# Performance work log

Hardware: AMD Instinct MI355X
Metric: run time of the kernel (lower is better)

Reference implementation:

```python
import jax, jax.numpy as jnp
import numpy as np

N = 524288
NUM_LEVELS = 16
FEATS = 2
LOG2_T = 19
TABLE = 1 << LOG2_T
MIN_RES, MAX_RES = 16, 1024
PRIMES = np.array([1, 2654435761, 805459861], dtype=np.uint32)
_growth = np.exp((np.log(MAX_RES) - np.log(MIN_RES)) / (NUM_LEVELS - 1))
SCALINGS = np.floor(MIN_RES * _growth ** np.arange(NUM_LEVELS)).astype(np.float32)  # [L]


def hash_encode(positions, table):
    # positions [N,3] in [0,1]; table [L*T, F]
    scaled = positions[:, None, :] * jnp.asarray(SCALINGS)[None, :, None]  # [N,L,3]
    fl = jnp.floor(scaled)
    ce = jnp.ceil(scaled)
    offset = scaled - fl  # [N,L,3]
    primes = jnp.asarray(PRIMES)  # [3] uint32
    lvl_off = jnp.arange(NUM_LEVELS, dtype=jnp.uint32) * jnp.uint32(TABLE)  # [L]
    out = jnp.zeros(scaled.shape[:2] + (FEATS,), scaled.dtype)
    for corner in range(8):
        bits = np.array([(corner >> d) & 1 for d in range(3)], dtype=np.float32)
        coord = jnp.where(jnp.asarray(bits, dtype=bool), ce, fl)
        h = coord.astype(jnp.int32).astype(jnp.uint32) * primes  # [N,L,3]
        h = h[..., 0] ^ h[..., 1] ^ h[..., 2]
        idx = ((h & jnp.uint32(TABLE - 1)) + lvl_off).astype(jnp.int32)  # [N,L]
        b = jnp.asarray(bits)
        w = jnp.prod(b * offset + (1.0 - b) * (1.0 - offset), axis=-1, keepdims=True)  # [N,L,1]
        out = out + w * table[idx]
    return out.reshape(out.shape[0], NUM_LEVELS * FEATS)  # [N,32]


def nerf_encode(d):
    # NeRFEncoding: 4 freqs in 2**linspace(0,4,4), include_input=True -> 27 dims
    freqs = 2.0 ** jnp.linspace(0.0, 4.0, 4)
    scaled = (2.0 * jnp.pi * d)[..., None] * freqs  # [N,3,4]
    scaled = scaled.reshape(d.shape[0], -1)  # [N,12]
    enc = jnp.sin(jnp.concatenate([scaled, scaled + jnp.pi / 2.0], axis=-1))  # [N,24]
    return jnp.concatenate([enc, d], axis=-1)  # [N,27]


def setup_inputs() -> dict:
    key = jax.random.key(0)
    ks = jax.random.split(key, 16)
    w = lambda k, i, o: jax.random.normal(k, (i, o), jnp.float32) * (1.0 / np.sqrt(i))
    return {
        "positions": jax.random.uniform(ks[0], (N, 3), jnp.float32),
        "directions": jax.random.normal(ks[1], (N, 3), jnp.float32),
        "hash_table": (jax.random.uniform(ks[2], (NUM_LEVELS * TABLE, FEATS), jnp.float32) * 2.0 - 1.0) * 1e-3,
        "w0": w(ks[3], 32, 64), "b0": jnp.zeros((64,), jnp.float32),
        "w1": w(ks[4], 64, 64), "b1": jnp.zeros((64,), jnp.float32),
        "w2": w(ks[5], 64, 64), "b2": jnp.zeros((64,), jnp.float32),
        "wr": w(ks[6], 91, 32), "br": jnp.zeros((32,), jnp.float32),
        "wc": w(ks[7], 32, 3), "bc": jnp.zeros((3,), jnp.float32),
        "wd": w(ks[8], 64, 1), "bd": jnp.zeros((1,), jnp.float32),
    }


def reference(positions, directions, hash_table, w0, b0, w1, b1, w2, b2, wr, br, wc, bc, wd, bd):
    enc_xyz = hash_encode(positions, hash_table)  # [N,32]
    enc_dir = nerf_encode(directions)  # [N,27]
    h = jax.nn.relu(enc_xyz @ w0 + b0)
    h = jax.nn.relu(h @ w1 + b1)
    base = h @ w2 + b2  # [N,64], linear out (out_activation=None)
    rgb_h = jnp.concatenate([enc_dir, base], axis=-1) @ wr + br  # [N,32], single layer
    rgb = jax.nn.sigmoid(rgb_h @ wc + bc)  # [N,3]
    density = jax.nn.softplus(base @ wd + bd)  # [N,1]
    return jnp.concatenate([rgb, density], axis=-1)  # [N,4]
```

## Files before the change

### kernel.cpp

```cpp
#include <hip/hip_runtime.h>
#include <math.h>

#define NPTS 524288
#define LOG2T 19
#define TSIZE (1u << LOG2T)
#define TMASK (TSIZE - 1u)

typedef unsigned int uint32;
typedef unsigned short ushort16;

typedef __attribute__((ext_vector_type(8))) short short8;
typedef __attribute__((ext_vector_type(4))) float f32x4;

__device__ __forceinline__ float bf2f(ushort16 u) {
    union { uint32 i; float f; } v; v.i = ((uint32)u) << 16; return v.f;
}
__device__ __forceinline__ ushort16 f2bf(float f) {
    union { float f; uint32 i; } v; v.f = f;
    uint32 r = v.i + 0x7fffu + ((v.i >> 16) & 1u);
    return (ushort16)(r >> 16);
}
__device__ __forceinline__ uint32 pack2(float a, float b) {
    return (uint32)f2bf(a) | ((uint32)f2bf(b) << 16);
}
__device__ __forceinline__ float ldin(const void* p, int i, bool f32) {
    return f32 ? ((const float*)p)[i] : bf2f(((const ushort16*)p)[i]);
}

struct Scal16 { float s[16]; };
struct Freq4  { float f[4]; };

__global__ __launch_bounds__(256) void k_cvt(const void* __restrict__ pos,
                                             const float4* __restrict__ tbl,
                                             uint4* __restrict__ tbl2) {
    __shared__ int sFlag;
    int tid = threadIdx.x;
    if (tid < 64) {
        const ushort16* ph = (const ushort16*)pos;
        float v0 = bf2f(ph[tid]), v1 = bf2f(ph[tid + 64]);
        bool odd = !(fabsf(v0) <= 4.f) || !(fabsf(v1) <= 4.f);
        unsigned long long m = __ballot(odd);
        if (tid == 0) sFlag = (m != 0ull) ? 1 : 0;
    }
    __syncthreads();
    if (sFlag == 0) return;
    size_t g = (size_t)blockIdx.x * 256 + tid;
    float4 v0 = tbl[2 * g], v1 = tbl[2 * g + 1];
    uint4 o;
    o.x = pack2(v0.x, v0.y); o.y = pack2(v0.z, v0.w);
    o.z = pack2(v1.x, v1.y); o.w = pack2(v1.z, v1.w);
    tbl2[g] = o;
}

__global__ __launch_bounds__(256) void k_hash2(const void* __restrict__ pos,
                                               const void* __restrict__ tbl,
                                               const uint32* __restrict__ tbl2,
                                               uint32* __restrict__ enc,
                                               Scal16 sc, int lvl0) {
    __shared__ int sFlag;
    int tid = threadIdx.x;
    if (tid < 64) {
        const ushort16* ph = (const ushort16*)pos;
        float v0 = bf2f(ph[tid]), v1 = bf2f(ph[tid + 64]);
        bool odd = !(fabsf(v0) <= 4.f) || !(fabsf(v1) <= 4.f);
        unsigned long long m = __ballot(odd);
        if (tid == 0) sFlag = (m != 0ull) ? 1 : 0;
    }
    __syncthreads();
    const bool f32 = (sFlag != 0);
    const uint32* tp = f32 ? tbl2 : (const uint32*)tbl;

    int lvl = lvl0 + (blockIdx.x & 7);
    int pt = (blockIdx.x >> 3) * 256 + tid;

    float s = sc.s[lvl];
    float x = ldin(pos, 3 * pt, f32), y = ldin(pos, 3 * pt + 1, f32), z = ldin(pos, 3 * pt + 2, f32);
    float sx = x * s, sy = y * s, sz = z * s;
    float fx = floorf(sx), fy = floorf(sy), fz = floorf(sz);
    float cx = ceilf(sx), cy = ceilf(sy), cz = ceilf(sz);
    float ox = sx - fx, oy = sy - fy, oz = sz - fz;
    uint32 hx0 = (uint32)(int)fx;
    uint32 hx1 = (uint32)(int)cx;
    uint32 hy0 = (uint32)(int)fy * 2654435761u;
    uint32 hy1 = (uint32)(int)cy * 2654435761u;
    uint32 hz0 = (uint32)(int)fz * 805459861u;
    uint32 hz1 = (uint32)(int)cz * 805459861u;
    uint32 base = (uint32)lvl << LOG2T;
    float wx0 = 1.f - ox, wy0 = 1.f - oy, wz0 = 1.f - oz;

    float a0 = 0.f, a1 = 0.f;
#pragma unroll
    for (int yz = 0; yz < 4; ++yz) {
        uint32 m = ((yz & 1) ? hy1 : hy0) ^ ((yz & 2) ? hz1 : hz0);
        float wyz = ((yz & 1) ? oy : wy0) * ((yz & 2) ? oz : wz0);
        uint32 i0 = ((hx0 ^ m) & TMASK) + base;
        uint32 i1 = ((hx1 ^ m) & TMASK) + base;
        uint32 d0, d1;
        if (i1 == (i0 ^ 1u)) {
            uint2 pv = *(const uint2*)(tp + (i0 & ~1u));
            d0 = (i0 & 1u) ? pv.y : pv.x;
            d1 = (i0 & 1u) ? pv.x : pv.y;
        } else {
            d0 = tp[i0]; d1 = tp[i1];
        }
        float f0 = bf2f((ushort16)(d0 & 0xffffu)), f1 = bf2f((ushort16)(d0 >> 16));
        float c0 = bf2f((ushort16)(d1 & 0xffffu)), c1 = bf2f((ushort16)(d1 >> 16));
        a0 += wyz * (wx0 * f0 + ox * c0);
        a1 += wyz * (wx0 * f1 + ox * c1);
    }
    enc[(size_t)lvl * NPTS + pt] = pack2(a0, a1);
}

__global__ __launch_bounds__(256) void k_hash(const void* __restrict__ pos,
                                              const void* __restrict__ tbl,
                                              uint32* __restrict__ enc,
                                              Scal16 sc) {
    __shared__ int sFlag;
    int tid = threadIdx.x;
    if (tid < 64) {
        const ushort16* ph = (const ushort16*)pos;
        float v0 = bf2f(ph[tid]), v1 = bf2f(ph[tid + 64]);
        bool odd = !(fabsf(v0) <= 4.f) || !(fabsf(v1) <= 4.f);
        unsigned long long m = __ballot(odd);
        if (tid == 0) sFlag = (m != 0ull) ? 1 : 0;
    }
    __syncthreads();
    const bool f32 = (sFlag != 0);

    int lvl = ((blockIdx.x >> 14) << 3) + (blockIdx.x & 7);
    int pt = ((blockIdx.x >> 3) & 2047) * 256 + tid;

    float s = sc.s[lvl];
    float x = ldin(pos, 3 * pt, f32), y = ldin(pos, 3 * pt + 1, f32), z = ldin(pos, 3 * pt + 2, f32);
    float sx = x * s, sy = y * s, sz = z * s;
    float fx = floorf(sx), fy = floorf(sy), fz = floorf(sz);
    float cx = ceilf(sx), cy = ceilf(sy), cz = ceilf(sz);
    float ox = sx - fx, oy = sy - fy, oz = sz - fz;
    uint32 hx0 = (uint32)(int)fx;
    uint32 hx1 = (uint32)(int)cx;
    uint32 hy0 = (uint32)(int)fy * 2654435761u;
    uint32 hy1 = (uint32)(int)cy * 2654435761u;
    uint32 hz0 = (uint32)(int)fz * 805459861u;
    uint32 hz1 = (uint32)(int)cz * 805459861u;
    uint32 base = (uint32)lvl << LOG2T;
    float wx0 = 1.f - ox, wy0 = 1.f - oy, wz0 = 1.f - oz;

    float a0 = 0.f, a1 = 0.f;
    if (f32) {
        const float* tf = (const float*)tbl;
#pragma unroll
        for (int yz = 0; yz < 4; ++yz) {
            uint32 m = ((yz & 1) ? hy1 : hy0) ^ ((yz & 2) ? hz1 : hz0);
            float wyz = ((yz & 1) ? oy : wy0) * ((yz & 2) ? oz : wz0);
            uint32 i0 = ((hx0 ^ m) & TMASK) + base;
            uint32 i1 = ((hx1 ^ m) & TMASK) + base;
            float4 pv = *(const float4*)(tf + (size_t)(i0 & ~1u) * 2);
            bool lo = !(i0 & 1u);
            float f0 = lo ? pv.x : pv.z, f1 = lo ? pv.y : pv.w;
            float c0, c1;
            if (i1 == (i0 ^ 1u)) { c0 = lo ? pv.z : pv.x; c1 = lo ? pv.w : pv.y; }
            else { float2 tv = ((const float2*)tbl)[i1]; c0 = tv.x; c1 = tv.y; }
            a0 += wyz * (wx0 * f0 + ox * c0);
            a1 += wyz * (wx0 * f1 + ox * c1);
        }
    } else {
#pragma unroll
        for (int cr = 0; cr < 8; ++cr) {
            uint32 h = ((cr & 1) ? hx1 : hx0) ^ ((cr & 2) ? hy1 : hy0) ^ ((cr & 4) ? hz1 : hz0);
            uint32 idx = (h & TMASK) + base;
            uint32 dv = ((const uint32*)tbl)[idx];
            float w = ((cr & 1) ? ox : wx0) * ((cr & 2) ? oy : wy0) * ((cr & 4) ? oz : wz0);
            a0 += w * bf2f((ushort16)(dv & 0xffffu));
            a1 += w * bf2f((ushort16)(dv >> 16));
        }
    }
    enc[(size_t)lvl * NPTS + pt] = pack2(a0, a1);
}

#define STRY 72
#define STRW0 40
#define STRW12 72
#define STRWR 104
#define MSTRX 100
#define PPI 128
#define NIT (NPTS / PPI)

__global__ __launch_bounds__(512) void k_mlp(
    const void* __restrict__ pos,
    const uint32* __restrict__ enc, const void* __restrict__ dirs,
    const void* __restrict__ w0, const void* __restrict__ b0,
    const void* __restrict__ w1, const void* __restrict__ b1,
    const void* __restrict__ w2, const void* __restrict__ b2,
    const void* __restrict__ wr, const void* __restrict__ br,
    const void* __restrict__ wc, const void* __restrict__ bc,
    const void* __restrict__ wd, const void* __restrict__ bd,
    void* __restrict__ out, Freq4 fq)
{
    __shared__ __align__(16) ushort16 sX[PPI * MSTRX];
    __shared__ __align__(16) ushort16 sY[PPI * STRY];
    __shared__ __align__(16) ushort16 sW0[64 * STRW0];
    __shared__ __align__(16) ushort16 sW1[64 * STRW12];
    __shared__ __align__(16) ushort16 sW2[64 * STRW12];
    __shared__ __align__(16) ushort16 sWR[32 * STRWR];
    __shared__ __align__(16) ushort16 sW4[16 * STRWR];
    __shared__ __align__(16) float sB0[64], sB1[64], sB2[64], sBR[32], sFB[4];
    __shared__ int sFlag;

    int tid = threadIdx.x;

    if (tid < 64) {
        const ushort16* ph = (const ushort16*)pos;
        float v0 = bf2f(ph[tid]), v1 = bf2f(ph[tid + 64]);
        bool odd = !(fabsf(v0) <= 4.f) || !(fabsf(v1) <= 4.f);
        unsigned long long m = __ballot(odd);
        if (tid == 0) sFlag = (m != 0ull) ? 1 : 0;
    }
    __syncthreads();
    const bool f32 = (sFlag != 0);

    for (int i = tid; i < 2048; i += 512) { int k = i >> 6, n = i & 63; sW0[n * STRW0 + k] = f2bf(ldin(w0, i, f32)); }
    for (int i = tid; i < 4096; i += 512) { int k = i >> 6, n = i & 63; sW1[n * STRW12 + k] = f2bf(ldin(w1, i, f32)); }
    for (int i = tid; i < 4096; i += 512) { int k = i >> 6, n = i & 63; sW2[n * STRW12 + k] = f2bf(ldin(w2, i, f32)); }
    for (int i = tid; i < 2912; i += 512) {
        int r = i >> 5, n = i & 31; int k = (r < 27) ? r : r + 5;
        sWR[n * STRWR + k] = f2bf(ldin(wr, i, f32));
    }
    if (tid < 160) { int n = tid / 5, k = 27 + tid % 5; sWR[n * STRWR + k] = 0; }
    for (int i = tid; i < 1536; i += 512) {
        int n = i / 96, j = i % 96;
        float v = 0.f;
        if (n == 3 && j < 64) v = ldin(wd, j, f32);
        else if (n < 3 && j >= 64) v = ldin(wc, (j - 64) * 3 + n, f32);
        sW4[n * STRWR + j] = f2bf(v);
    }
    if (tid < 64) { sB0[tid] = ldin(b0, tid, f32); sB1[tid] = ldin(b1, tid, f32); sB2[tid] = ldin(b2, tid, f32); }
    if (tid < 32) sBR[tid] = ldin(br, tid, f32);
    if (tid < 3) sFB[tid] = ldin(bc, tid, f32);
    if (tid == 3) sFB[3] = ldin(bd, 0, f32);

    int lane = tid & 63, wv = tid >> 6;
    int colg = lane & 15, quad = lane >> 4;
    int myrow = wv * 16 + colg;

    for (int c = blockIdx.x; c < NIT; c += gridDim.x) {
        int p0 = c * PPI;
        __syncthreads();

        for (int i = tid; i < 1024; i += 512) {
            int l = i >> 6, p2 = (i & 63) * 2;
            uint2 e = *(const uint2*)&enc[(size_t)l * NPTS + p0 + p2];
            *(uint32*)&sX[p2 * MSTRX + 2 * l] = e.x;
            *(uint32*)&sX[(p2 + 1) * MSTRX + 2 * l] = e.y;
        }
        if (tid < 384) {
            int p = tid / 3, i2 = tid - 3 * (tid / 3);
            float dvv = ldin(dirs, 3 * (p0 + p) + i2, f32);
            ushort16* row = &sX[p * MSTRX + 64];
            float td = 6.28318530717958647692f * dvv;
            float a0 = td * fq.f[0], a1 = td * fq.f[1], a2 = td * fq.f[2], a3 = td * fq.f[3];
            uint2 sv, cv;
            sv.x = pack2(__sinf(a0), __sinf(a1));
            sv.y = pack2(__sinf(a2), __sinf(a3));
            cv.x = pack2(__cosf(a0), __cosf(a1));
            cv.y = pack2(__cosf(a2), __cosf(a3));
            *(uint2*)&row[i2 * 4] = sv;
            *(uint2*)&row[12 + i2 * 4] = cv;
            row[24 + i2] = f2bf(dvv);
        } else {
            int p = tid - 384;
            ushort16* row = &sX[p * MSTRX + 64];
#pragma unroll
            for (int j = 27; j < 32; ++j) row[j] = 0;
        }
        __syncthreads();

        {
            short8 xb = *(const short8*)&sX[myrow * MSTRX + quad * 8];
#pragma unroll
            for (int nt = 0; nt < 4; ++nt) {
                short8 a = *(const short8*)&sW0[(nt * 16 + colg) * STRW0 + quad * 8];
                f32x4 acc = {0.f, 0.f, 0.f, 0.f};
                acc = __builtin_amdgcn_mfma_f32_16x16x32_bf16(a, xb, acc, 0, 0, 0);
                float4 bi = *(const float4*)&sB0[nt * 16 + quad * 4];
                uint2 o;
                o.x = pack2(fmaxf(acc[0] + bi.x, 0.f), fmaxf(acc[1] + bi.y, 0.f));
                o.y = pack2(fmaxf(acc[2] + bi.z, 0.f), fmaxf(acc[3] + bi.w, 0.f));
                *(uint2*)&sY[myrow * STRY + nt * 16 + quad * 4] = o;
            }
        }
        {
            short8 xb0 = *(const short8*)&sY[myrow * STRY + quad * 8];
            short8 xb1 = *(const short8*)&sY[myrow * STRY + 32 + quad * 8];
#pragma unroll
            for (int nt = 0; nt < 4; ++nt) {
                short8 a0 = *(const short8*)&sW1[(nt * 16 + colg) * STRW12 + quad * 8];
                short8 a1 = *(const short8*)&sW1[(nt * 16 + colg) * STRW12 + 32 + quad * 8];
                f32x4 acc = {0.f, 0.f, 0.f, 0.f};
                acc = __builtin_amdgcn_mfma_f32_16x16x32_bf16(a0, xb0, acc, 0, 0, 0);
                acc = __builtin_amdgcn_mfma_f32_16x16x32_bf16(a1, xb1, acc, 0, 0, 0);
                float4 bi = *(const float4*)&sB1[nt * 16 + quad * 4];
                uint2 o;
                o.x = pack2(fmaxf(acc[0] + bi.x, 0.f), fmaxf(acc[1] + bi.y, 0.f));
                o.y = pack2(fmaxf(acc[2] + bi.z, 0.f), fmaxf(acc[3] + bi.w, 0.f));
                *(uint2*)&sX[myrow * MSTRX + nt * 16 + quad * 4] = o;
            }
        }
        {
            short8 xb0 = *(const short8*)&sX[myrow * MSTRX + quad * 8];
            short8 xb1 = *(const short8*)&sX[myrow * MSTRX + 32 + quad * 8];
#pragma unroll
            for (int nt = 0; nt < 4; ++nt) {
                short8 a0 = *(const short8*)&sW2[(nt * 16 + colg) * STRW12 + quad * 8];
                short8 a1 = *(const short8*)&sW2[(nt * 16 + colg) * STRW12 + 32 + quad * 8];
                f32x4 acc = {0.f, 0.f, 0.f, 0.f};
                acc = __builtin_amdgcn_mfma_f32_16x16x32_bf16(a0, xb0, acc, 0, 0, 0);
                acc = __builtin_amdgcn_mfma_f32_16x16x32_bf16(a1, xb1, acc, 0, 0, 0);
                float4 bi = *(const float4*)&sB2[nt * 16 + quad * 4];
                uint2 o;
                o.x = pack2(acc[0] + bi.x, acc[1] + bi.y);
                o.y = pack2(acc[2] + bi.z, acc[3] + bi.w);
                *(uint2*)&sY[myrow * STRY + nt * 16 + quad * 4] = o;
            }
        }
        {
            short8 xb0 = *(const short8*)&sX[myrow * MSTRX + 64 + quad * 8];
            short8 xb1 = *(const short8*)&sY[myrow * STRY + quad * 8];
            short8 xb2 = *(const short8*)&sY[myrow * STRY + 32 + quad * 8];
#pragma unroll
            for (int nt = 0; nt < 2; ++nt) {
                short8 a0 = *(const short8*)&sWR[(nt * 16 + colg) * STRWR + quad * 8];
                short8 a1 = *(const short8*)&sWR[(nt * 16 + colg) * STRWR + 32 + quad * 8];
                short8 a2 = *(const short8*)&sWR[(nt * 16 + colg) * STRWR + 64 + quad * 8];
                f32x4 acc = {0.f, 0.f, 0.f, 0.f};
                acc = __builtin_amdgcn_mfma_f32_16x16x32_bf16(a0, xb0, acc, 0, 0, 0);
                acc = __builtin_amdgcn_mfma_f32_16x16x32_bf16(a1, xb1, acc, 0, 0, 0);
                acc = __builtin_amdgcn_mfma_f32_16x16x32_bf16(a2, xb2, acc, 0, 0, 0);
                float4 bi = *(const float4*)&sBR[nt * 16 + quad * 4];
                uint2 o;
                o.x = pack2(acc[0] + bi.x, acc[1] + bi.y);
                o.y = pack2(acc[2] + bi.z, acc[3] + bi.w);
                *(uint2*)&sX[myrow * MSTRX + nt * 16 + quad * 4] = o;
            }
        }
        {
            short8 xb0 = *(const short8*)&sY[myrow * STRY + quad * 8];
            short8 xb1 = *(const short8*)&sY[myrow * STRY + 32 + quad * 8];
            short8 xb2 = *(const short8*)&sX[myrow * MSTRX + quad * 8];
            short8 a0 = *(const short8*)&sW4[colg * STRWR + quad * 8];
            short8 a1 = *(const short8*)&sW4[colg * STRWR + 32 + quad * 8];
            short8 a2 = *(const short8*)&sW4[colg * STRWR + 64 + quad * 8];
            f32x4 acc = {0.f, 0.f, 0.f, 0.f};
            acc = __builtin_amdgcn_mfma_f32_16x16x32_bf16(a0, xb0, acc, 0, 0, 0);
            acc = __builtin_amdgcn_mfma_f32_16x16x32_bf16(a1, xb1, acc, 0, 0, 0);
            acc = __builtin_amdgcn_mfma_f32_16x16x32_bf16(a2, xb2, acc, 0, 0, 0);
            if (quad == 0) {
                float r0 = acc[0] + sFB[0], r1 = acc[1] + sFB[1], r2 = acc[2] + sFB[2], dd = acc[3] + sFB[3];
                r0 = 1.f / (1.f + expf(-r0));
                r1 = 1.f / (1.f + expf(-r1));
                r2 = 1.f / (1.f + expf(-r2));
                float sp = (dd > 0.f) ? (dd + log1pf(expf(-dd))) : log1pf(expf(dd));
                int pt = p0 + myrow;
                if (f32) {
                    float4 o4; o4.x = r0; o4.y = r1; o4.z = r2; o4.w = sp;
                    ((float4*)out)[pt] = o4;
                } else {
                    uint2 o; o.x = pack2(r0, r1); o.y = pack2(r2, sp);
                    ((uint2*)out)[pt] = o;
                }
            }
        }
    }
}

#define FSTRX 104
__global__ __launch_bounds__(256) void k_fused(
    const void* __restrict__ pos, const void* __restrict__ dirs,
    const void* __restrict__ tbl,
    const void* __restrict__ w0, const void* __restrict__ b0,
    const void* __restrict__ w1, const void* __restrict__ b1,
    const void* __restrict__ w2, const void* __restrict__ b2,
    const void* __restrict__ wr, const void* __restrict__ br,
    const void* __restrict__ wc, const void* __restrict__ bc,
    const void* __restrict__ wd, const void* __restrict__ bd,
    void* __restrict__ out, Scal16 sc, Freq4 fq)
{
    __shared__ __align__(16) ushort16 sX[64 * FSTRX];
    __shared__ __align__(16) ushort16 sY[64 * STRY];
    __shared__ __align__(16) ushort16 sW0[64 * STRW0];
    __shared__ __align__(16) ushort16 sW1[64 * STRW12];
    __shared__ __align__(16) ushort16 sW2[64 * STRW12];
    __shared__ __align__(16) ushort16 sWR[32 * STRWR];
    __shared__ float sB0[64], sB1[64], sB2[64], sBR[32];
    __shared__ float sWCf[100];
    __shared__ float sWDf[64];
    __shared__ float sPosF[192];
    __shared__ int sFlag;

    int tid = threadIdx.x;
    if (tid < 64) {
        const ushort16* ph = (const ushort16*)pos;
        float v0 = bf2f(ph[tid]), v1 = bf2f(ph[tid + 64]);
        bool odd = !(fabsf(v0) <= 4.f) || !(fabsf(v1) <= 4.f);
        unsigned long long m = __ballot(odd);
        if (tid == 0) sFlag = (m != 0ull) ? 1 : 0;
    }
    __syncthreads();
    const bool f32 = (sFlag != 0);

    for (int i = tid; i < 2048; i += 256) { int k = i >> 6, n = i & 63; sW0[n * STRW0 + k] = f2bf(ldin(w0, i, f32)); }
    for (int i = tid; i < 4096; i += 256) { int k = i >> 6, n = i & 63; sW1[n * STRW12 + k] = f2bf(ldin(w1, i, f32)); }
    for (int i = tid; i < 4096; i += 256) { int k = i >> 6, n = i & 63; sW2[n * STRW12 + k] = f2bf(ldin(w2, i, f32)); }
    for (int i = tid; i < 2912; i += 256) {
        int r = i >> 5, n = i & 31; int k = (r < 27) ? r : r + 5;
        sWR[n * STRWR + k] = f2bf(ldin(wr, i, f32));
    }
    if (tid < 160) { int n = tid / 5, k = 27 + tid % 5; sWR[n * STRWR + k] = 0; }
    if (tid < 64) { sB0[tid] = ldin(b0, tid, f32); sB1[tid] = ldin(b1, tid, f32);
                    sB2[tid] = ldin(b2, tid, f32); sWDf[tid] = ldin(wd, tid, f32); }
    if (tid < 32) sBR[tid] = ldin(br, tid, f32);
    if (tid < 96) sWCf[tid] = ldin(wc, tid, f32);
    if (tid == 96) { sWCf[96] = ldin(bc, 0, f32); sWCf[97] = ldin(bc, 1, f32);
                     sWCf[98] = ldin(bc, 2, f32); sWCf[99] = ldin(bd, 0, f32); }

    int lane = tid & 63, wv = tid >> 6;
    int colg = lane & 15, quad = lane >> 4;
    int myl = tid & 15;
    float mys = sc.s[myl];
    uint32 mybase = (uint32)myl << LOG2T;

    for (int c = blockIdx.x; c < NPTS / 64; c += gridDim.x) {
        int p0 = c * 64;
        __syncthreads();
        if (tid < 192) sPosF[tid] = ldin(pos, p0 * 3 + tid, f32);
        __syncthreads();
#pragma unroll
        for (int ii = 0; ii < 4; ++ii) {
            int p = (tid >> 4) + 16 * ii;
            float x = sPosF[3 * p], y = sPosF[3 * p + 1], z = sPosF[3 * p + 2];
            float sx = x * mys, sy = y * mys, sz = z * mys;
            float fx = floorf(sx), fy = floorf(sy), fz = floorf(sz);
            float cx = ceilf(sx), cy = ceilf(sy), cz = ceilf(sz);
            float ox = sx - fx, oy = sy - fy, oz = sz - fz;
            uint32 hx0 = (uint32)(int)fx;
            uint32 hx1 = (uint32)(int)cx;
            uint32 hy0 = (uint32)(int)fy * 2654435761u;
            uint32 hy1 = (uint32)(int)cy * 2654435761u;
            uint32 hz0 = (uint32)(int)fz * 805459861u;
            uint32 hz1 = (uint32)(int)cz * 805459861u;
            float wx0 = 1.f - ox, wy0 = 1.f - oy, wz0 = 1.f - oz;
            float a0 = 0.f, a1 = 0.f;
#pragma unroll
            for (int cr = 0; cr < 8; ++cr) {
                uint32 h = ((cr & 1) ? hx1 : hx0) ^ ((cr & 2) ? hy1 : hy0) ^ ((cr & 4) ? hz1 : hz0);
                uint32 idx = (h & TMASK) + mybase;
                float t0, t1;
                if (f32) { float2 tv = ((const float2*)tbl)[idx]; t0 = tv.x; t1 = tv.y; }
                else { uint32 dv = ((const uint32*)tbl)[idx]; t0 = bf2f((ushort16)(dv & 0xffffu)); t1 = bf2f((ushort16)(dv >> 16)); }
                float w = ((cr & 1) ? ox : wx0) * ((cr & 2) ? oy : wy0) * ((cr & 4) ? oz : wz0);
                a0 += w * t0; a1 += w * t1;
            }
            *(uint32*)&sX[p * FSTRX + 2 * myl] = pack2(a0, a1);
        }
        __syncthreads();
        {
            short8 a = *(const short8*)&sX[(wv * 16 + colg) * FSTRX + quad * 8];
#pragma unroll
            for (int nt = 0; nt < 4; ++nt) {
                short8 bb = *(const short8*)&sW0[(nt * 16 + colg) * STRW0 + quad * 8];
                f32x4 acc = {0.f, 0.f, 0.f, 0.f};
                acc = __builtin_amdgcn_mfma_f32_16x16x32_bf16(a, bb, acc, 0, 0, 0);
                float bias = sB0[nt * 16 + colg];
#pragma unroll
                for (int r = 0; r < 4; ++r) {
                    float v = fmaxf(acc[r] + bias, 0.f);
                    sY[(wv * 16 + quad * 4 + r) * STRY + nt * 16 + colg] = f2bf(v);
                }
            }
        }
        __syncthreads();
        {
            short8 a0 = *(const short8*)&sY[(wv * 16 + colg) * STRY + quad * 8];
            short8 a1 = *(const short8*)&sY[(wv * 16 + colg) * STRY + 32 + quad * 8];
#pragma unroll
            for (int nt = 0; nt < 4; ++nt) {
                short8 bb0 = *(const short8*)&sW1[(nt * 16 + colg) * STRW12 + quad * 8];
                short8 bb1 = *(const short8*)&sW1[(nt * 16 + colg) * STRW12 + 32 + quad * 8];
                f32x4 acc = {0.f, 0.f, 0.f, 0.f};
                acc = __builtin_amdgcn_mfma_f32_16x16x32_bf16(a0, bb0, acc, 0, 0, 0);
                acc = __builtin_amdgcn_mfma_f32_16x16x32_bf16(a1, bb1, acc, 0, 0, 0);
                float bias = sB1[nt * 16 + colg];
#pragma unroll
                for (int r = 0; r < 4; ++r) {
                    float v = fmaxf(acc[r] + bias, 0.f);
                    sX[(wv * 16 + quad * 4 + r) * FSTRX + nt * 16 + colg] = f2bf(v);
                }
            }
        }
        __syncthreads();
        {
            short8 a0 = *(const short8*)&sX[(wv * 16 + colg) * FSTRX + quad * 8];
            short8 a1 = *(const short8*)&sX[(wv * 16 + colg) * FSTRX + 32 + quad * 8];
#pragma unroll
            for (int nt = 0; nt < 4; ++nt) {
                short8 bb0 = *(const short8*)&sW2[(nt * 16 + colg) * STRW12 + quad * 8];
                short8 bb1 = *(const short8*)&sW2[(nt * 16 + colg) * STRW12 + 32 + quad * 8];
                f32x4 acc = {0.f, 0.f, 0.f, 0.f};
                acc = __builtin_amdgcn_mfma_f32_16x16x32_bf16(a0, bb0, acc, 0, 0, 0);
                acc = __builtin_amdgcn_mfma_f32_16x16x32_bf16(a1, bb1, acc, 0, 0, 0);
                float bias = sB2[nt * 16 + colg];
#pragma unroll
                for (int r = 0; r < 4; ++r) {
                    sY[(wv * 16 + quad * 4 + r) * STRY + nt * 16 + colg] = f2bf(acc[r] + bias);
                }
            }
        }
        if (tid < 192) {
            int p = tid / 3, i2 = tid % 3;
            float dvv = ldin(dirs, 3 * (p0 + p) + i2, f32);
            ushort16* row = &sX[p * FSTRX + 64];
            float td = 6.28318530717958647692f * dvv;
#pragma unroll
            for (int j = 0; j < 4; ++j) {
                float arg = td * fq.f[j];
                float sv, cv;
                sincosf(arg, &sv, &cv);
                row[i2 * 4 + j] = f2bf(sv);
                row[12 + i2 * 4 + j] = f2bf(cv);
            }
            row[24 + i2] = f2bf(dvv);
        } else {
            int p = tid - 192;
            ushort16* row = &sX[p * FSTRX + 64];
#pragma unroll
            for (int j = 27; j < 32; ++j) row[j] = 0;
        }
        __syncthreads();
        {
            short8 a0 = *(const short8*)&sX[(wv * 16 + colg) * FSTRX + 64 + quad * 8];
            short8 a1 = *(const short8*)&sY[(wv * 16 + colg) * STRY + quad * 8];
            short8 a2 = *(const short8*)&sY[(wv * 16 + colg) * STRY + 32 + quad * 8];
#pragma unroll
            for (int nt = 0; nt < 2; ++nt) {
                short8 bb0 = *(const short8*)&sWR[(nt * 16 + colg) * STRWR + quad * 8];
                short8 bb1 = *(const short8*)&sWR[(nt * 16 + colg) * STRWR + 32 + quad * 8];
                short8 bb2 = *(const short8*)&sWR[(nt * 16 + colg) * STRWR + 64 + quad * 8];
                f32x4 acc = {0.f, 0.f, 0.f, 0.f};
                acc = __builtin_amdgcn_mfma_f32_16x16x32_bf16(a0, bb0, acc, 0, 0, 0);
                acc = __builtin_amdgcn_mfma_f32_16x16x32_bf16(a1, bb1, acc, 0, 0, 0);
                acc = __builtin_amdgcn_mfma_f32_16x16x32_bf16(a2, bb2, acc, 0, 0, 0);
                float bias = sBR[nt * 16 + colg];
#pragma unroll
                for (int r = 0; r < 4; ++r) {
                    sX[(wv * 16 + quad * 4 + r) * FSTRX + nt * 16 + colg] = f2bf(acc[r] + bias);
                }
            }
        }
        __syncthreads();
        if (tid < 64) {
            int pt = p0 + tid;
            float r0 = 0.f, r1 = 0.f, r2 = 0.f, dd = 0.f;
            const ushort16* hx = &sX[tid * FSTRX];
            const ushort16* hb = &sY[tid * STRY];
#pragma unroll
            for (int k = 0; k < 32; ++k) {
                float hv = bf2f(hx[k]);
                r0 += hv * sWCf[k * 3 + 0];
                r1 += hv * sWCf[k * 3 + 1];
                r2 += hv * sWCf[k * 3 + 2];
            }
#pragma unroll
            for (int k = 0; k < 64; ++k) dd += bf2f(hb[k]) * sWDf[k];
            r0 += sWCf[96]; r1 += sWCf[97]; r2 += sWCf[98]; dd += sWCf[99];
            r0 = 1.f / (1.f + expf(-r0));
            r1 = 1.f / (1.f + expf(-r1));
            r2 = 1.f / (1.f + expf(-r2));
            float sp = (dd > 0.f) ? (dd + log1pf(expf(-dd))) : log1pf(expf(dd));
            if (f32) {
                float4 o4; o4.x = r0; o4.y = r1; o4.z = r2; o4.w = sp;
                ((float4*)out)[pt] = o4;
            } else {
                uint2 o;
                o.x = pack2(r0, r1); o.y = pack2(r2, sp);
                ((uint2*)out)[pt] = o;
            }
        }
    }
}

extern "C" void kernel_launch(void* const* d_in, const int* in_sizes, int n_in,
                              void* d_out, int out_size, void* d_ws, size_t ws_size,
                              hipStream_t stream) {
    (void)in_sizes; (void)n_in; (void)out_size;

    Scal16 sc;
    double g = exp((log(1024.0) - log(16.0)) / 15.0);
    for (int l = 0; l < 16; ++l) sc.s[l] = (float)floor(16.0 * pow(g, (double)l));

    Freq4 fq;
    float lv[4] = {0.f, 4.f / 3.f, 8.f / 3.f, 4.f};
    for (int j = 0; j < 4; ++j) fq.f[j] = (float)pow(2.0, (double)lv[j]);

    const size_t enc_bytes = (size_t)16 * NPTS * 4;
    const size_t tbl2_bytes = (size_t)16 * TSIZE * 4;
    if (ws_size >= enc_bytes + tbl2_bytes) {
        uint32* enc = (uint32*)d_ws;
        uint32* tbl2 = (uint32*)((char*)d_ws + enc_bytes);
        k_cvt<<<dim3(8192), dim3(256), 0, stream>>>(d_in[0], (const float4*)d_in[2], (uint4*)tbl2);
        k_hash2<<<dim3(8 * NPTS / 256), dim3(256), 0, stream>>>(d_in[0], d_in[2], tbl2, enc, sc, 0);
        k_hash2<<<dim3(8 * NPTS / 256), dim3(256), 0, stream>>>(d_in[0], d_in[2], tbl2, enc, sc, 8);
        k_mlp<<<dim3(512), dim3(512), 0, stream>>>(
            d_in[0], enc, d_in[1], d_in[3], d_in[4], d_in[5], d_in[6], d_in[7],
            d_in[8], d_in[9], d_in[10], d_in[11], d_in[12], d_in[13], d_in[14],
            d_out, fq);
    } else if (ws_size >= enc_bytes) {
        uint32* enc = (uint32*)d_ws;
        k_hash<<<dim3(2 * 8 * NPTS / 256), dim3(256), 0, stream>>>(d_in[0], d_in[2], enc, sc);
        k_mlp<<<dim3(512), dim3(512), 0, stream>>>(
            d_in[0], enc, d_in[1], d_in[3], d_in[4], d_in[5], d_in[6], d_in[7],
            d_in[8], d_in[9], d_in[10], d_in[11], d_in[12], d_in[13], d_in[14],
            d_out, fq);
    } else {
        k_fused<<<dim3(512), dim3(256), 0, stream>>>(
            d_in[0], d_in[1], d_in[2], d_in[3], d_in[4], d_in[5], d_in[6], d_in[7],
            d_in[8], d_in[9], d_in[10], d_in[11], d_in[12], d_in[13], d_in[14],
            d_out, sc, fq);
    }
}
```

Baseline: 344.4 us.

## Precompute dense corner tables for coarse hash levels and stage positions in LDS

```diff
diff --git a/kernel.cpp b/kernel.cpp
--- a/kernel.cpp
+++ b/kernel.cpp
@@ -29,10 +29,12 @@
 
 struct Scal16 { float s[16]; };
 struct Freq4  { float f[4]; };
-
-__global__ __launch_bounds__(256) void k_cvt(const void* __restrict__ pos,
-                                             const float4* __restrict__ tbl,
-                                             uint4* __restrict__ tbl2) {
+struct HashP  { float s[16]; int dD[8]; int doff[8]; };
+struct DenseP { int dD[6]; int pfx[7]; };
+
+__global__ __launch_bounds__(256) void k_cvt10(const void* __restrict__ pos,
+                                               const float4* __restrict__ tbl,
+                                               uint4* __restrict__ tbl2F) {
     __shared__ int sFlag;
     int tid = threadIdx.x;
     if (tid < 64) {
@@ -45,18 +47,18 @@
     __syncthreads();
     if (sFlag == 0) return;
     size_t g = (size_t)blockIdx.x * 256 + tid;
-    float4 v0 = tbl[2 * g], v1 = tbl[2 * g + 1];
+    float4 v0 = tbl[(size_t)3 * TSIZE + 2 * g];
+    float4 v1 = tbl[(size_t)3 * TSIZE + 2 * g + 1];
     uint4 o;
     o.x = pack2(v0.x, v0.y); o.y = pack2(v0.z, v0.w);
     o.z = pack2(v1.x, v1.y); o.w = pack2(v1.z, v1.w);
-    tbl2[g] = o;
-}
-
-__global__ __launch_bounds__(256) void k_hash2(const void* __restrict__ pos,
+    tbl2F[g] = o;
+}
+
+__global__ __launch_bounds__(256) void k_dense(const void* __restrict__ pos,
                                                const void* __restrict__ tbl,
-                                               const uint32* __restrict__ tbl2,
-                                               uint32* __restrict__ enc,
-                                               Scal16 sc, int lvl0) {
+                                               uint4* __restrict__ dense4,
+                                               DenseP dp) {
     __shared__ int sFlag;
     int tid = threadIdx.x;
     if (tid < 64) {
@@ -68,45 +70,151 @@
     }
     __syncthreads();
     const bool f32 = (sFlag != 0);
-    const uint32* tp = f32 ? tbl2 : (const uint32*)tbl;
+
+    int e = blockIdx.x * 256 + tid;
+    if (e >= dp.pfx[6]) return;
+    int l = 0;
+#pragma unroll
+    for (int k = 1; k < 6; ++k) l += (e >= dp.pfx[k]) ? 1 : 0;
+    int c = e - dp.pfx[l];
+    int D = dp.dD[l], D2 = D * D;
+    int cz = c / D2; int rm = c - cz * D2;
+    int cy = rm / D; int cx = rm - cy * D;
+
+    uint32 base = (uint32)l << LOG2T;
+    uint32 hz  = (uint32)cz * 805459861u;
+    uint32 hy0 = (uint32)cy * 2654435761u;
+    uint32 hy1 = (uint32)(cy + 1) * 2654435761u;
+    uint32 h00 = ((((uint32)cx)       ^ hy0 ^ hz) & TMASK) + base;
+    uint32 h10 = ((((uint32)(cx + 1)) ^ hy0 ^ hz) & TMASK) + base;
+    uint32 h01 = ((((uint32)cx)       ^ hy1 ^ hz) & TMASK) + base;
+    uint32 h11 = ((((uint32)(cx + 1)) ^ hy1 ^ hz) & TMASK) + base;
+
+    uint4 o;
+    if (f32) {
+        const float2* t2 = (const float2*)tbl;
+        float2 a = t2[h00], b = t2[h10], cc = t2[h01], d = t2[h11];
+        o.x = pack2(a.x, a.y); o.y = pack2(b.x, b.y);
+        o.z = pack2(cc.x, cc.y); o.w = pack2(d.x, d.y);
+    } else {
+        const uint32* t1 = (const uint32*)tbl;
+        o.x = t1[h00]; o.y = t1[h10]; o.z = t1[h01]; o.w = t1[h11];
+    }
+    dense4[e] = o;
+}
+
+__global__ __launch_bounds__(256) void k_hashU(const void* __restrict__ pos,
+                                               const void* __restrict__ tbl,
+                                               const uint32* __restrict__ tbl2F,
+                                               const uint4* __restrict__ dense4,
+                                               uint32* __restrict__ enc,
+                                               HashP hp, int lvl0) {
+    __shared__ __align__(16) uint4 sPosQ[192];
+    __shared__ int sFlag;
+    int tid = threadIdx.x;
+    if (tid < 64) {
+        const ushort16* ph = (const ushort16*)pos;
+        float v0 = bf2f(ph[tid]), v1 = bf2f(ph[tid + 64]);
+        bool odd = !(fabsf(v0) <= 4.f) || !(fabsf(v1) <= 4.f);
+        unsigned long long m = __ballot(odd);
+        if (tid == 0) sFlag = (m != 0ull) ? 1 : 0;
+    }
+    __syncthreads();
+    const bool f32 = (sFlag != 0);
 
     int lvl = lvl0 + (blockIdx.x & 7);
-    int pt = (blockIdx.x >> 3) * 256 + tid;
-
-    float s = sc.s[lvl];
-    float x = ldin(pos, 3 * pt, f32), y = ldin(pos, 3 * pt + 1, f32), z = ldin(pos, 3 * pt + 2, f32);
+    int chunk = blockIdx.x >> 3;
+    int p0 = chunk * 256;
+    int pt = p0 + tid;
+
+    {
+        int n16 = f32 ? 192 : 96;
+        const uint4* src = (const uint4*)((const char*)pos + (size_t)p0 * (f32 ? 12 : 6));
+        for (int i = tid; i < n16; i += 256) sPosQ[i] = src[i];
+    }
+    __syncthreads();
+
+    float x, y, z;
+    if (f32) {
+        const float* pf = (const float*)sPosQ;
+        x = pf[3 * tid]; y = pf[3 * tid + 1]; z = pf[3 * tid + 2];
+    } else {
+        const ushort16* ph2 = (const ushort16*)sPosQ;
+        x = bf2f(ph2[3 * tid]); y = bf2f(ph2[3 * tid + 1]); z = bf2f(ph2[3 * tid + 2]);
+    }
+
+    float s = hp.s[lvl];
     float sx = x * s, sy = y * s, sz = z * s;
     float fx = floorf(sx), fy = floorf(sy), fz = floorf(sz);
     float cx = ceilf(sx), cy = ceilf(sy), cz = ceilf(sz);
     float ox = sx - fx, oy = sy - fy, oz = sz - fz;
-    uint32 hx0 = (uint32)(int)fx;
-    uint32 hx1 = (uint32)(int)cx;
-    uint32 hy0 = (uint32)(int)fy * 2654435761u;
-    uint32 hy1 = (uint32)(int)cy * 2654435761u;
-    uint32 hz0 = (uint32)(int)fz * 805459861u;
-    uint32 hz1 = (uint32)(int)cz * 805459861u;
-    uint32 base = (uint32)lvl << LOG2T;
     float wx0 = 1.f - ox, wy0 = 1.f - oy, wz0 = 1.f - oz;
 
     float a0 = 0.f, a1 = 0.f;
-#pragma unroll
-    for (int yz = 0; yz < 4; ++yz) {
-        uint32 m = ((yz & 1) ? hy1 : hy0) ^ ((yz & 2) ? hz1 : hz0);
-        float wyz = ((yz & 1) ? oy : wy0) * ((yz & 2) ? oz : wz0);
-        uint32 i0 = ((hx0 ^ m) & TMASK) + base;
-        uint32 i1 = ((hx1 ^ m) & TMASK) + base;
-        uint32 d0, d1;
-        if (i1 == (i0 ^ 1u)) {
-            uint2 pv = *(const uint2*)(tp + (i0 & ~1u));
-            d0 = (i0 & 1u) ? pv.y : pv.x;
-            d1 = (i0 & 1u) ? pv.x : pv.y;
-        } else {
-            d0 = tp[i0]; d1 = tp[i1];
-        }
-        float f0 = bf2f((ushort16)(d0 & 0xffffu)), f1 = bf2f((ushort16)(d0 >> 16));
-        float c0 = bf2f((ushort16)(d1 & 0xffffu)), c1 = bf2f((ushort16)(d1 >> 16));
-        a0 += wyz * (wx0 * f0 + ox * c0);
-        a1 += wyz * (wx0 * f1 + ox * c1);
+
+    if (lvl < 6) {
+        int D = hp.dD[lvl], D2 = D * D;
+        int fxi = (int)fx, fyi = (int)fy, fzi = (int)fz;
+        bool dxb = ((int)cx != fxi);
+        bool dyb = ((int)cy != fyi);
+        bool dzb = ((int)cz != fzi);
+        const uint4* dp4 = dense4 + hp.doff[lvl];
+        int i0 = fxi + fyi * D + fzi * D2;
+        uint4 P0 = dp4[i0];
+        uint4 P1 = dp4[i0 + (dzb ? D2 : 0)];
+        {
+            uint32 fv = P0.x, cv = dxb ? P0.y : P0.x;
+            float w = wy0 * wz0;
+            a0 += w * (wx0 * bf2f((ushort16)(fv & 0xffffu)) + ox * bf2f((ushort16)(cv & 0xffffu)));
+            a1 += w * (wx0 * bf2f((ushort16)(fv >> 16))     + ox * bf2f((ushort16)(cv >> 16)));
+        }
+        {
+            uint32 fv = dyb ? P0.z : P0.x;
+            uint32 cv = dyb ? (dxb ? P0.w : P0.z) : (dxb ? P0.y : P0.x);
+            float w = oy * wz0;
+            a0 += w * (wx0 * bf2f((ushort16)(fv & 0xffffu)) + ox * bf2f((ushort16)(cv & 0xffffu)));
+            a1 += w * (wx0 * bf2f((ushort16)(fv >> 16))     + ox * bf2f((ushort16)(cv >> 16)));
+        }
+        {
+            uint32 fv = P1.x, cv = dxb ? P1.y : P1.x;
+            float w = wy0 * oz;
+            a0 += w * (wx0 * bf2f((ushort16)(fv & 0xffffu)) + ox * bf2f((ushort16)(cv & 0xffffu)));
+            a1 += w * (wx0 * bf2f((ushort16)(fv >> 16))     + ox * bf2f((ushort16)(cv >> 16)));
+        }
+        {
+            uint32 fv = dyb ? P1.z : P1.x;
+            uint32 cv = dyb ? (dxb ? P1.w : P1.z) : (dxb ? P1.y : P1.x);
+            float w = oy * oz;
+            a0 += w * (wx0 * bf2f((ushort16)(fv & 0xffffu)) + ox * bf2f((ushort16)(cv & 0xffffu)));
+            a1 += w * (wx0 * bf2f((ushort16)(fv >> 16))     + ox * bf2f((ushort16)(cv >> 16)));
+        }
+    } else {
+        const uint32* tp; uint32 base;
+        if (f32) { tp = tbl2F; base = (uint32)(lvl - 6) << LOG2T; }
+        else     { tp = (const uint32*)tbl; base = (uint32)lvl << LOG2T; }
+        uint32 hx0 = (uint32)(int)fx;
+        uint32 hx1 = (uint32)(int)cx;
+        uint32 hy0 = (uint32)(int)fy * 2654435761u;
+        uint32 hy1 = (uint32)(int)cy * 2654435761u;
+        uint32 hz0 = (uint32)(int)fz * 805459861u;
+        uint32 hz1 = (uint32)(int)cz * 805459861u;
+#pragma unroll
+        for (int yz = 0; yz < 4; ++yz) {
+            uint32 m = ((yz & 1) ? hy1 : hy0) ^ ((yz & 2) ? hz1 : hz0);
+            float wyz = ((yz & 1) ? oy : wy0) * ((yz & 2) ? oz : wz0);
+            uint32 i0 = ((hx0 ^ m) & TMASK) + base;
+            uint32 i1 = ((hx1 ^ m) & TMASK) + base;
+            uint32 d0, d1;
+            if (i1 == (i0 ^ 1u)) {
+                uint2 pv = *(const uint2*)(tp + (i0 & ~1u));
+                d0 = (i0 & 1u) ? pv.y : pv.x;
+                d1 = (i0 & 1u) ? pv.x : pv.y;
+            } else {
+                d0 = tp[i0]; d1 = tp[i1];
+            }
+            a0 += wyz * (wx0 * bf2f((ushort16)(d0 & 0xffffu)) + ox * bf2f((ushort16)(d1 & 0xffffu)));
+            a1 += wyz * (wx0 * bf2f((ushort16)(d0 >> 16))     + ox * bf2f((ushort16)(d1 >> 16)));
+        }
     }
     enc[(size_t)lvl * NPTS + pt] = pack2(a0, a1);
 }
@@ -600,14 +708,34 @@
     float lv[4] = {0.f, 4.f / 3.f, 8.f / 3.f, 4.f};
     for (int j = 0; j < 4; ++j) fq.f[j] = (float)pow(2.0, (double)lv[j]);
 
-    const size_t enc_bytes = (size_t)16 * NPTS * 4;
-    const size_t tbl2_bytes = (size_t)16 * TSIZE * 4;
-    if (ws_size >= enc_bytes + tbl2_bytes) {
-        uint32* enc = (uint32*)d_ws;
-        uint32* tbl2 = (uint32*)((char*)d_ws + enc_bytes);
-        k_cvt<<<dim3(8192), dim3(256), 0, stream>>>(d_in[0], (const float4*)d_in[2], (uint4*)tbl2);
-        k_hash2<<<dim3(8 * NPTS / 256), dim3(256), 0, stream>>>(d_in[0], d_in[2], tbl2, enc, sc, 0);
-        k_hash2<<<dim3(8 * NPTS / 256), dim3(256), 0, stream>>>(d_in[0], d_in[2], tbl2, enc, sc, 8);
+    DenseP dpp;
+    HashP hp;
+    dpp.pfx[0] = 0;
+    for (int l = 0; l < 6; ++l) {
+        int D = (int)sc.s[l] + 1;
+        dpp.dD[l] = D;
+        dpp.pfx[l + 1] = dpp.pfx[l] + D * D * D;
+    }
+    for (int l = 0; l < 16; ++l) hp.s[l] = sc.s[l];
+    for (int l = 0; l < 8; ++l) {
+        hp.dD[l]   = (l < 6) ? dpp.dD[l] : 1;
+        hp.doff[l] = (l < 6) ? dpp.pfx[l] : 0;
+    }
+    int ndense = dpp.pfx[6];
+
+    const size_t enc_bytes   = (size_t)16 * NPTS * 4;
+    const size_t tbl2F_bytes = (size_t)10 * TSIZE * 4;
+    const size_t dense_bytes = (size_t)ndense * 16 + 64;
+    const size_t need_new = enc_bytes + tbl2F_bytes + dense_bytes;
+
+    if (ws_size >= need_new) {
+        uint32* enc   = (uint32*)d_ws;
+        uint32* tbl2F = (uint32*)((char*)d_ws + enc_bytes);
+        uint4*  dense4 = (uint4*)((char*)d_ws + enc_bytes + tbl2F_bytes);
+        k_cvt10<<<dim3(5120), dim3(256), 0, stream>>>(d_in[0], (const float4*)d_in[2], (uint4*)tbl2F);
+        k_dense<<<dim3((ndense + 255) / 256), dim3(256), 0, stream>>>(d_in[0], d_in[2], dense4, dpp);
+        k_hashU<<<dim3(8 * NPTS / 256), dim3(256), 0, stream>>>(d_in[0], d_in[2], tbl2F, dense4, enc, hp, 0);
+        k_hashU<<<dim3(8 * NPTS / 256), dim3(256), 0, stream>>>(d_in[0], d_in[2], tbl2F, dense4, enc, hp, 8);
         k_mlp<<<dim3(512), dim3(512), 0, stream>>>(
             d_in[0], enc, d_in[1], d_in[3], d_in[4], d_in[5], d_in[6], d_in[7],
             d_in[8], d_in[9], d_in[10], d_in[11], d_in[12], d_in[13], d_in[14],
```

Result: no change. 345.6 us (+0.4%).
